# Performance work log

Hardware: AMD Instinct MI355X
Metric: run time of the kernel (lower is better)

The kernel has to match this reference:

```python
import jax, jax.numpy as jnp
import numpy as np

H = 1024

def gru_step(x, h, W_ih, W_hh, b_ih, b_hh):
    # torch.nn.GRUCell math; gate order r, z, n
    gi = x @ W_ih.T + b_ih            # [N, 3H]
    gh = h @ W_hh.T + b_hh            # [N, 3H]
    i_r, i_z, i_n = jnp.split(gi, 3, axis=-1)
    h_r, h_z, h_n = jnp.split(gh, 3, axis=-1)
    r = jax.nn.sigmoid(i_r + h_r)
    z = jax.nn.sigmoid(i_z + h_z)
    n = jnp.tanh(i_n + r * h_n)
    return (1.0 - z) * n + z * h


def setup_inputs() -> dict:
    key = jax.random.key(0)
    ks = jax.random.split(key, 12)
    V, Nr, Na = 256, 4096, 4096
    s = 1.0 / np.sqrt(H)
    return {
        'state': jax.random.normal(ks[0], (1, H), jnp.float32),
        'rel_tokens': jax.random.randint(ks[1], (Nr, 3), 0, V, jnp.int32),
        'attr_tokens': jax.random.randint(ks[2], (Na, 2), 0, V, jnp.int32),
        'table': jax.random.normal(ks[3], (V, H), jnp.float32),
        'W_emb': jax.random.normal(ks[4], (H, H), jnp.float32) * s,
        'b_emb': jnp.zeros((H,), jnp.float32),
        'W_ih': jax.random.normal(ks[5], (3 * H, H), jnp.float32) * s,
        'W_hh': jax.random.normal(ks[6], (3 * H, H), jnp.float32) * s,
        'b_ih': jnp.zeros((3 * H,), jnp.float32),
        'b_hh': jnp.zeros((3 * H,), jnp.float32),
        'W1': jax.random.normal(ks[7], (H, H), jnp.float32) * s,
        'b1': jnp.zeros((H,), jnp.float32),
        'W2': jax.random.normal(ks[8], (H, H), jnp.float32) * s,
        'b2': jnp.zeros((H,), jnp.float32),
        'W3': jax.random.normal(ks[9], (1, H), jnp.float32) * s,
        'b3': jnp.zeros((1,), jnp.float32),
        'eps': jax.random.uniform(ks[10], (1,), jnp.float32) * 0.1,
    }


def reference(state, rel_tokens, attr_tokens, table, W_emb, b_emb,
              W_ih, W_hh, b_ih, b_hh, W1, b1, W2, b2, W3, b3, eps):
    Nr, Na = rel_tokens.shape[0], attr_tokens.shape[0]
    # per-clause token embeddings passed through embedding_layer (Linear)
    rel_e = jnp.einsum('nte,he->nth', table[rel_tokens], W_emb) + b_emb   # [Nr,3,H]
    att_e = jnp.einsum('nte,he->nth', table[attr_tokens], W_emb) + b_emb  # [Na,2,H]

    # relation clauses: 3 chained GRU steps from global state
    h = jnp.broadcast_to(state, (Nr, H))
    for t in range(3):
        h = gru_step(rel_e[:, t], h, W_ih, W_hh, b_ih, b_hh)
    rel_h = h
    # attribute clauses: 2 chained GRU steps from global state
    h = jnp.broadcast_to(state, (Na, H))
    for t in range(2):
        h = gru_step(att_e[:, t], h, W_ih, W_hh, b_ih, b_hh)
    attr_h = h

    clause = jnp.concatenate([rel_h, attr_h], axis=0)          # [N, H]
    x = jax.nn.relu(clause @ W1.T + b1)
    x = jax.nn.relu(x @ W2.T + b2)
    logits = (x @ W3.T + b3).reshape(1, -1)                    # [1, N]
    probs = jax.nn.softmax(logits, axis=1)                     # softmax over clauses
    n = jnp.float32(probs.shape[1])
    probs = probs * (1.0 - eps[0]) + eps[0] / n                # eps smoothing
    return probs
```

## Files before the change

### kernel.cpp

```cpp
#include <hip/hip_runtime.h>
#include <math.h>

#define H 1024
#define H3 3072
#define NVOC 256

typedef __attribute__((ext_vector_type(8))) short bf16x8;
typedef __attribute__((ext_vector_type(4))) float f32x4;

__device__ __forceinline__ float sigf(float x) { return 1.0f / (1.0f + expf(-x)); }

__device__ __forceinline__ unsigned short f2bf(float f) {
    unsigned int u = __float_as_uint(f);
    u = (u + 0x7fffu + ((u >> 16) & 1u)) >> 16;
    return (unsigned short)u;
}
__device__ __forceinline__ float bf2f(unsigned short u) {
    return __uint_as_float(((unsigned int)u) << 16);
}

#define MM256(MH, AV, BV)                                                          \
    __builtin_amdgcn_s_setprio(1);                                                 \
    _Pragma("unroll")                                                              \
    for (int m_ = 0; m_ < 4; ++m_)                                                 \
        _Pragma("unroll")                                                          \
        for (int n_ = 0; n_ < 4; ++n_)                                             \
            acc[(MH) * 4 + m_][n_] = __builtin_amdgcn_mfma_f32_16x16x32_bf16(      \
                AV[m_], BV[n_], acc[(MH) * 4 + m_][n_], 0, 0, 0);                  \
    __builtin_amdgcn_s_setprio(0);

#define RDA256(BUF, MH, KQ)                                                        \
    _Pragma("unroll")                                                              \
    for (int m_ = 0; m_ < 4; ++m_)                                                 \
        a[m_] = *reinterpret_cast<const bf16x8*>(                                  \
            ldsb + (BUF) * 65536 + (g * 128 + (MH) * 64 + m_ * 16 + fr) * 128 +    \
            (((KQ) * 4 + fq) ^ (fr & 7)) * 16);

#define RDB256(BUF, KQ, DST)                                                       \
    _Pragma("unroll")                                                              \
    for (int n_ = 0; n_ < 4; ++n_)                                                 \
        DST[n_] = *reinterpret_cast<const bf16x8*>(                                \
            ldsb + (BUF) * 65536 + 32768 + (wn + n_ * 16 + fr) * 128 +             \
            (((KQ) * 4 + fq) ^ (fr & 7)) * 16);

#define BAR256() __builtin_amdgcn_s_barrier()

template<bool RELU, int OUT_MODE>
__global__ __launch_bounds__(512, 2)
void gemm256(const unsigned short* __restrict__ A, const unsigned short* __restrict__ W,
             const float* __restrict__ bias, void* __restrict__ C,
             int N, int K, int gx,
             const float* __restrict__ w3, float* __restrict__ logits)
{
    __shared__ unsigned short lds[65536];
    char* ldsb = (char*)lds;
    const int tid = threadIdx.x;
    const int wid = tid >> 6, lane = tid & 63;

    const int nwg = gridDim.x;
    const int cpx = nwg >> 3;
    const int bid = blockIdx.x;
    const int swz = (bid & 7) * cpx + (bid >> 3);
    const int bm = (swz / gx) * 256;
    const int bn = (swz % gx) * 256;

    const int g = wid >> 2;
    const int wn = (wid & 3) * 64;
    const int fr = lane & 15, fq = lane >> 4;

    const int sr = tid >> 3;
    const int sc = ((tid & 7) ^ (sr & 7)) * 8;
    auto stage_unit = [&](int t, int u) {
        const unsigned short* src = (u < 4)
            ? A + (size_t)(bm + u * 64 + sr) * K + t * 64 + sc
            : W + (size_t)(bn + (u - 4) * 64 + sr) * K + t * 64 + sc;
        char* dst = ldsb + (t & 1) * 65536 + u * 8192 + tid * 16;
        __builtin_amdgcn_global_load_lds(
            (const __attribute__((address_space(1))) void*)src,
            (__attribute__((address_space(3))) void*)dst, 16, 0, 0);
    };

    f32x4 acc[8][4];
#pragma unroll
    for (int i = 0; i < 8; i++)
#pragma unroll
        for (int j = 0; j < 4; j++) acc[i][j] = (f32x4){0.f, 0.f, 0.f, 0.f};
    bf16x8 a[4], b0[4], b1[4];

    const int nt = K >> 6;

#pragma unroll
    for (int u = 0; u < 8; ++u) stage_unit(0, u);
    stage_unit(1, 0); stage_unit(1, 2); stage_unit(1, 4);
    stage_unit(1, 5); stage_unit(1, 6); stage_unit(1, 7);
    asm volatile("s_waitcnt vmcnt(6)" ::: "memory");
    __builtin_amdgcn_sched_barrier(0);
    BAR256();

    for (int t = 0; t < nt; ++t) {
        const int buf = t & 1;
        RDB256(buf, 0, b0); RDA256(buf, 0, 0);
        if (t + 1 < nt) stage_unit(t + 1, 1);
        MM256(0, a, b0); BAR256();
        RDB256(buf, 1, b1); RDA256(buf, 0, 1);
        if (t + 1 < nt) stage_unit(t + 1, 3);
        MM256(0, a, b1); BAR256();
        RDA256(buf, 1, 0);
        if (t + 2 < nt) { stage_unit(t + 2, 0); stage_unit(t + 2, 2); stage_unit(t + 2, 4); }
        MM256(1, a, b0); BAR256();
        RDA256(buf, 1, 1);
        if (t + 2 < nt) { stage_unit(t + 2, 5); stage_unit(t + 2, 6); stage_unit(t + 2, 7); }
        MM256(1, a, b1);
        if (t + 2 < nt) {
            asm volatile("s_waitcnt vmcnt(6)" ::: "memory");
            __builtin_amdgcn_sched_barrier(0);
        } else if (t + 1 < nt) {
            asm volatile("s_waitcnt vmcnt(0)" ::: "memory");
            __builtin_amdgcn_sched_barrier(0);
        }
        BAR256();
    }

    if (OUT_MODE == 2) {
        float rs[8][4];
#pragma unroll
        for (int m = 0; m < 8; m++)
#pragma unroll
            for (int j = 0; j < 4; j++) rs[m][j] = 0.f;
#pragma unroll
        for (int n = 0; n < 4; n++) {
            const int col = bn + wn + n * 16 + fr;
            const float bv = bias[col];
            const float wv = w3[col];
#pragma unroll
            for (int m = 0; m < 8; m++)
#pragma unroll
                for (int j = 0; j < 4; j++) {
                    float v = acc[m][n][j] + bv;
                    if (RELU) v = fmaxf(v, 0.f);
                    rs[m][j] = fmaf(v, wv, rs[m][j]);
                }
        }
#pragma unroll
        for (int m = 0; m < 8; m++)
#pragma unroll
            for (int j = 0; j < 4; j++) {
                float s = rs[m][j];
                s += __shfl_xor(s, 1); s += __shfl_xor(s, 2);
                s += __shfl_xor(s, 4); s += __shfl_xor(s, 8);
                if (fr == 0) {
                    const int row = bm + g * 128 + (m >> 2) * 64 + (m & 3) * 16 + fq * 4 + j;
                    atomicAdd(logits + row, s);
                }
            }
    } else {
#pragma unroll
        for (int m = 0; m < 8; m++) {
#pragma unroll
            for (int n = 0; n < 4; n++) {
                const int col = bn + wn + n * 16 + fr;
                const float bv = bias[col];
#pragma unroll
                for (int j = 0; j < 4; j++) {
                    const int row = bm + g * 128 + (m >> 2) * 64 + (m & 3) * 16 + fq * 4 + j;
                    float v = acc[m][n][j] + bv;
                    if (RELU) v = fmaxf(v, 0.f);
                    ((unsigned short*)C)[(size_t)row * N + col] = f2bf(v);
                }
            }
        }
    }
}

template<bool RELU, int OUT_MODE>
__global__ __launch_bounds__(256)
void gemm_bf16(const unsigned short* __restrict__ A, const unsigned short* __restrict__ W,
               const float* __restrict__ bias, void* __restrict__ C,
               int N, int K, int gx, int Kc,
               const float* __restrict__ w3, float* __restrict__ logits)
{
    __shared__ unsigned short As[4][128 * 32];
    __shared__ unsigned short Ws[4][128 * 32];
    const int tid = threadIdx.x;
    const int wid = tid >> 6, lane = tid & 63;

    const int nwg = gridDim.x;
    const int cpx = nwg >> 3;
    const int bid = blockIdx.x;
    const int swz = (bid & 7) * cpx + (bid >> 3);
    const int bm = (swz / gx) * 128;
    const int bn = (swz % gx) * 128;
    const int k_base = blockIdx.y * Kc;
    const int nt = Kc >> 5;

    const int wm = (wid >> 1) * 64, wn = (wid & 1) * 64;
    const int fr = lane & 15;
    const int fq = lane >> 4;
    const int perm = fq ^ (fr & 3);

    f32x4 acc[4][4];
#pragma unroll
    for (int i = 0; i < 4; i++)
#pragma unroll
        for (int j = 0; j < 4; j++) acc[i][j] = (f32x4){0.f, 0.f, 0.f, 0.f};

    const int srow = tid >> 2;
    const int schunk = (tid & 3) ^ (srow & 3);
    const unsigned short* aS = A + (size_t)(bm + srow) * K + k_base + schunk * 8;
    const unsigned short* wS = W + (size_t)(bn + srow) * K + k_base + schunk * 8;
    const size_t rstep = (size_t)64 * K;

    auto stage = [&](int b, int t) {
        const unsigned short* a0 = aS + t * 32;
        const unsigned short* w0 = wS + t * 32;
        __builtin_amdgcn_global_load_lds(
            (const __attribute__((address_space(1))) void*)a0,
            (__attribute__((address_space(3))) void*)(&As[b][wid * 512]), 16, 0, 0);
        __builtin_amdgcn_global_load_lds(
            (const __attribute__((address_space(1))) void*)(a0 + rstep),
            (__attribute__((address_space(3))) void*)(&As[b][2048 + wid * 512]), 16, 0, 0);
        __builtin_amdgcn_global_load_lds(
            (const __attribute__((address_space(1))) void*)w0,
            (__attribute__((address_space(3))) void*)(&Ws[b][wid * 512]), 16, 0, 0);
        __builtin_amdgcn_global_load_lds(
            (const __attribute__((address_space(1))) void*)(w0 + rstep),
            (__attribute__((address_space(3))) void*)(&Ws[b][2048 + wid * 512]), 16, 0, 0);
    };

    stage(0, 0);
    if (nt > 1) stage(1, 1);
    if (nt > 2) stage(2, 2);

    for (int t = 0; t < nt; ++t) {
        if (t + 2 < nt)      asm volatile("s_waitcnt vmcnt(8)" ::: "memory");
        else if (t + 1 < nt) asm volatile("s_waitcnt vmcnt(4)" ::: "memory");
        else                 asm volatile("s_waitcnt vmcnt(0)" ::: "memory");
        __builtin_amdgcn_s_barrier();
        __builtin_amdgcn_sched_barrier(0);
        if (t + 3 < nt) stage((t + 3) & 3, t + 3);

        const unsigned short* as = &As[t & 3][0];
        const unsigned short* ws = &Ws[t & 3][0];
        bf16x8 a[4], b[4];
#pragma unroll
        for (int m = 0; m < 4; m++)
            a[m] = *reinterpret_cast<const bf16x8*>(as + (wm + m * 16 + fr) * 32 + perm * 8);
#pragma unroll
        for (int n = 0; n < 4; n++)
            b[n] = *reinterpret_cast<const bf16x8*>(ws + (wn + n * 16 + fr) * 32 + perm * 8);
        __builtin_amdgcn_s_setprio(1);
#pragma unroll
        for (int m = 0; m < 4; m++)
#pragma unroll
            for (int n = 0; n < 4; n++)
                acc[m][n] = __builtin_amdgcn_mfma_f32_16x16x32_bf16(a[m], b[n], acc[m][n], 0, 0, 0);
        __builtin_amdgcn_s_setprio(0);
    }

    if (OUT_MODE == 3) {
        float* Cf = (float*)C;
#pragma unroll
        for (int m = 0; m < 4; m++)
#pragma unroll
            for (int n = 0; n < 4; n++) {
                const int col = bn + wn + n * 16 + fr;
#pragma unroll
                for (int j = 0; j < 4; j++) {
                    const int row = bm + wm + m * 16 + fq * 4 + j;
                    atomicAdd(Cf + (size_t)row * N + col, acc[m][n][j]);
                }
            }
    } else {
#pragma unroll
        for (int m = 0; m < 4; m++) {
#pragma unroll
            for (int n = 0; n < 4; n++) {
                const int col = bn + wn + n * 16 + fr;
                const float bv = bias[col];
#pragma unroll
                for (int j = 0; j < 4; j++) {
                    const int row = bm + wm + m * 16 + fq * 4 + j;
                    float v = acc[m][n][j] + bv;
                    if (RELU) v = fmaxf(v, 0.f);
                    if (OUT_MODE == 1)
                        ((unsigned short*)C)[(size_t)row * N + col] = f2bf(v);
                    else
                        ((float*)C)[(size_t)row * N + col] = v;
                }
            }
        }
    }
}

__global__ __launch_bounds__(256)
void prep(const float* __restrict__ W_hh, const float* __restrict__ W_ih,
          const float* __restrict__ W1, const float* __restrict__ W2,
          const float* __restrict__ W_emb, const float* __restrict__ table,
          const float* __restrict__ state, const float* __restrict__ b_emb,
          const float* __restrict__ b_ih, const float* __restrict__ b_hh,
          unsigned short* __restrict__ W_hhb, unsigned short* __restrict__ W_ihb,
          unsigned short* __restrict__ W1b, unsigned short* __restrict__ W2b,
          unsigned short* __restrict__ W_embb, unsigned short* __restrict__ tableb,
          float* __restrict__ gh0, float* __restrict__ emb32, float* __restrict__ Gi,
          float* __restrict__ gh1, float* __restrict__ logits)
{
    int b = blockIdx.x;
    const int t = threadIdx.x;
    if (b < 3072) {
        float4 w = *reinterpret_cast<const float4*>(W_hh + (size_t)b * H + t * 4);
        ushort4 o; o.x = f2bf(w.x); o.y = f2bf(w.y); o.z = f2bf(w.z); o.w = f2bf(w.w);
        *reinterpret_cast<ushort4*>(W_hhb + (size_t)b * H + t * 4) = o;
        float4 sv = *reinterpret_cast<const float4*>(state + t * 4);
        float s = w.x * sv.x + w.y * sv.y + w.z * sv.z + w.w * sv.w;
#pragma unroll
        for (int off = 32; off; off >>= 1) s += __shfl_down(s, off);
        __shared__ float ps[4];
        if ((t & 63) == 0) ps[t >> 6] = s;
        __syncthreads();
        if (t == 0) gh0[b] = ps[0] + ps[1] + ps[2] + ps[3] + b_hh[b];
        return;
    }
    b -= 3072;
    const float* src = nullptr; unsigned short* dst = nullptr;
    if (b < 3072)      { src = W_ih;  dst = W_ihb; }
    else if ((b -= 3072) < 1024) { src = W1; dst = W1b; }
    else if ((b -= 1024) < 1024) { src = W2; dst = W2b; }
    else if ((b -= 1024) < 1024) { src = W_emb; dst = W_embb; }
    else if ((b -= 1024) < 256)  { src = table; dst = tableb; }
    else {
        b -= 256;
        if (b < 256) {
            int i = b * 1024 + t * 4;
            *reinterpret_cast<float4*>(emb32 + i) =
                *reinterpret_cast<const float4*>(b_emb + (i & (H - 1)));
        } else if ((b -= 256) < 768) {
            int i = b * 1024 + t * 4;
            *reinterpret_cast<float4*>(Gi + i) =
                *reinterpret_cast<const float4*>(b_ih + i % H3);
        } else if ((b -= 768) < 768) {
            int i = b * 1024 + t * 4;
            *reinterpret_cast<float4*>(gh1 + i) =
                *reinterpret_cast<const float4*>(b_hh + i % H3);
        } else {
            b -= 768;
            int i = b * 1024 + t * 4;
            *reinterpret_cast<float4*>(logits + i) = (float4){0.f, 0.f, 0.f, 0.f};
        }
        return;
    }
    const int off = b * 1024 + t * 4;
    float4 v = *reinterpret_cast<const float4*>(src + off);
    ushort4 o; o.x = f2bf(v.x); o.y = f2bf(v.y); o.z = f2bf(v.z); o.w = f2bf(v.w);
    *reinterpret_cast<ushort4*>(dst + off) = o;
}

__global__ void cvt_emb(const float* __restrict__ in, unsigned short* __restrict__ out)
{
    int i = (blockIdx.x * blockDim.x + threadIdx.x) * 4;
    float4 v = *reinterpret_cast<const float4*>(in + i);
    ushort4 o;
    o.x = f2bf(v.x); o.y = f2bf(v.y); o.z = f2bf(v.z); o.w = f2bf(v.w);
    *reinterpret_cast<ushort4*>(out + i) = o;
}

__global__ void h1_combine(const float* __restrict__ Gi, const float* __restrict__ gh0,
                           const float* __restrict__ state, float* __restrict__ h1,
                           unsigned short* __restrict__ h1b)
{
    int idx = blockIdx.x * blockDim.x + threadIdx.x;
    int v = idx >> 10, h = idx & (H - 1);
    const float* g = Gi + (size_t)v * H3;
    float r = sigf(g[h] + gh0[h]);
    float z = sigf(g[H + h] + gh0[H + h]);
    float n = tanhf(fmaf(r, gh0[2 * H + h], g[2 * H + h]));
    float v2 = (1.f - z) * n + z * state[h];
    h1[idx] = v2;
    h1b[idx] = f2bf(v2);
}

__global__ void step2_both(const int* __restrict__ rel, const int* __restrict__ attr, int Nr,
                           const float* __restrict__ Gi, const float* __restrict__ gh1,
                           const float* __restrict__ h1,
                           unsigned short* __restrict__ h2b, unsigned short* __restrict__ attr_out)
{
    int idx = blockIdx.x * blockDim.x + threadIdx.x;
    int row = idx >> 10, h = idx & (H - 1);
    int t0, t1, orow = row;
    unsigned short* dst;
    if (row < Nr) { t0 = rel[row * 3 + 0]; t1 = rel[row * 3 + 1]; dst = h2b; }
    else { orow = row - Nr; t0 = attr[orow * 2 + 0]; t1 = attr[orow * 2 + 1]; dst = attr_out; }
    const float* g = Gi + (size_t)t1 * H3;
    const float* gh = gh1 + (size_t)t0 * H3;
    float r = sigf(g[h] + gh[h]);
    float z = sigf(g[H + h] + gh[H + h]);
    float n = tanhf(fmaf(r, gh[2 * H + h], g[2 * H + h]));
    float v = (1.f - z) * n + z * h1[(size_t)t0 * H + h];
    dst[(size_t)orow * H + h] = f2bf(v);
}

__global__ void step3_rel(const int* __restrict__ toks,
                          const float* __restrict__ Gi, const unsigned short* __restrict__ gh2b,
                          const unsigned short* __restrict__ h2b, unsigned short* __restrict__ outb)
{
    int idx = blockIdx.x * blockDim.x + threadIdx.x;
    int row = idx >> 10, h = idx & (H - 1);
    int t2 = toks[row * 3 + 2];
    const float* g = Gi + (size_t)t2 * H3;
    const unsigned short* gh = gh2b + (size_t)row * H3;
    float r = sigf(g[h] + bf2f(gh[h]));
    float z = sigf(g[H + h] + bf2f(gh[H + h]));
    float n = tanhf(fmaf(r, bf2f(gh[2 * H + h]), g[2 * H + h]));
    outb[idx] = f2bf((1.f - z) * n + z * bf2f(h2b[idx]));
}

__global__ void softmax_eps(const float* __restrict__ logits, const float* __restrict__ epsp,
                            float* __restrict__ out, int N)
{
    __shared__ float smax[16], ssum[16];
    int tid = threadIdx.x;
    int nw = blockDim.x >> 6;
    float m = -INFINITY;
    for (int i = tid; i < N; i += blockDim.x) m = fmaxf(m, logits[i]);
#pragma unroll
    for (int off = 32; off; off >>= 1) m = fmaxf(m, __shfl_down(m, off));
    if ((tid & 63) == 0) smax[tid >> 6] = m;
    __syncthreads();
    float M = smax[0];
    for (int i = 1; i < nw; i++) M = fmaxf(M, smax[i]);
    float s = 0.f;
    for (int i = tid; i < N; i += blockDim.x) s += expf(logits[i] - M);
#pragma unroll
    for (int off = 32; off; off >>= 1) s += __shfl_down(s, off);
    if ((tid & 63) == 0) ssum[tid >> 6] = s;
    __syncthreads();
    float S = 0.f;
    for (int i = 0; i < nw; i++) S += ssum[i];
    float e = epsp[0];
    float mul = (1.f - e) / S;
    float add = e / (float)N;
    for (int i = tid; i < N; i += blockDim.x) out[i] = expf(logits[i] - M) * mul + add;
}

extern "C" void kernel_launch(void* const* d_in, const int* in_sizes, int n_in,
                              void* d_out, int out_size, void* d_ws, size_t ws_size,
                              hipStream_t stream)
{
    const float* state       = (const float*)d_in[0];
    const int*   rel_tokens  = (const int*)d_in[1];
    const int*   attr_tokens = (const int*)d_in[2];
    const float* table       = (const float*)d_in[3];
    const float* W_emb       = (const float*)d_in[4];
    const float* b_emb       = (const float*)d_in[5];
    const float* W_ih        = (const float*)d_in[6];
    const float* W_hh        = (const float*)d_in[7];
    const float* b_ih        = (const float*)d_in[8];
    const float* b_hh        = (const float*)d_in[9];
    const float* W1          = (const float*)d_in[10];
    const float* b1          = (const float*)d_in[11];
    const float* W2          = (const float*)d_in[12];
    const float* b2          = (const float*)d_in[13];
    const float* W3          = (const float*)d_in[14];
    const float* eps         = (const float*)d_in[16];

    const int Nr = in_sizes[1] / 3;
    const int Na = in_sizes[2] / 2;
    const int Ntot = Nr + Na;

    float* ws     = (float*)d_ws;
    float* Gi     = ws;
    float* gh0    = Gi + NVOC * H3;
    float* h1     = gh0 + H3;
    float* gh1    = h1 + NVOC * H;
    float* emb32  = gh1 + NVOC * H3;
    float* logits = emb32 + NVOC * H;
    unsigned short* W_hhb   = (unsigned short*)(logits + Ntot);
    unsigned short* W_ihb   = W_hhb + (size_t)H3 * H;
    unsigned short* W1b     = W_ihb + (size_t)H3 * H;
    unsigned short* W2b     = W1b + (size_t)H * H;
    unsigned short* W_embb  = W2b + (size_t)H * H;
    unsigned short* tableb  = W_embb + (size_t)H * H;
    unsigned short* embb    = tableb + (size_t)NVOC * H;
    unsigned short* h1b     = embb + (size_t)NVOC * H;
    unsigned short* h2b     = h1b + (size_t)NVOC * H;
    unsigned short* gh2b    = h2b + (size_t)Nr * H;
    unsigned short* clauseb = gh2b + (size_t)Nr * H3;
    unsigned short* x1b     = clauseb + (size_t)Ntot * H;

    prep<<<11272, 256, 0, stream>>>(W_hh, W_ih, W1, W2, W_emb, table, state,
                                    b_emb, b_ih, b_hh,
                                    W_hhb, W_ihb, W1b, W2b, W_embb, tableb,
                                    gh0, emb32, Gi, gh1, logits);

    gemm_bf16<false, 3><<<dim3((H / 128) * (NVOC / 128), 4), 256, 0, stream>>>(
        tableb, W_embb, nullptr, emb32, H, H, H / 128, H / 4, nullptr, nullptr);
    cvt_emb<<<NVOC * H / 4 / 256, 256, 0, stream>>>(emb32, embb);
    gemm_bf16<false, 3><<<dim3((H3 / 128) * (NVOC / 128), 4), 256, 0, stream>>>(
        embb, W_ihb, nullptr, Gi, H3, H, H3 / 128, H / 4, nullptr, nullptr);
    h1_combine<<<NVOC * H / 256, 256, 0, stream>>>(Gi, gh0, state, h1, h1b);
    gemm_bf16<false, 3><<<dim3((H3 / 128) * (NVOC / 128), 4), 256, 0, stream>>>(
        h1b, W_hhb, nullptr, gh1, H3, H, H3 / 128, H / 4, nullptr, nullptr);
    step2_both<<<Ntot * (H / 256), 256, 0, stream>>>(rel_tokens, attr_tokens, Nr,
                                                     Gi, gh1, h1, h2b,
                                                     clauseb + (size_t)Nr * H);
    gemm256<false, 1><<<(Nr / 256) * (H3 / 256), 512, 0, stream>>>(
        h2b, W_hhb, b_hh, gh2b, H3, H, H3 / 256, nullptr, nullptr);
    step3_rel<<<Nr * (H / 256), 256, 0, stream>>>(rel_tokens, Gi, gh2b, h2b, clauseb);
    gemm256<true, 1><<<(Ntot / 256) * (H / 256), 512, 0, stream>>>(
        clauseb, W1b, b1, x1b, H, H, H / 256, nullptr, nullptr);
    gemm256<true, 2><<<(Ntot / 256) * (H / 256), 512, 0, stream>>>(
        x1b, W2b, b2, nullptr, H, H, H / 256, W3, logits);
    softmax_eps<<<1, 1024, 0, stream>>>(logits, eps, (float*)d_out, Ntot);
}
```

Baseline: 303.5 us.

## Add 128x256-tile triple-buffered GEMM for the MLP layers

Adds a new gemm_n kernel with 128x256 output tiles, a 64-wide K step, a three-stage LDS ring fed by direct global-to-LDS loads, and XOR-swizzled LDS layout. The two MLP GEMMs (W1 and W2 with the fused W3 logit reduction) now use it instead of the 256x256 gemm256. This doubles the workgroup count for these N=8192, H=1024 GEMMs, aiming to fill more CUs and overlap loads with MFMA. The cost is less reuse per tile and a larger LDS footprint per block.

```diff
diff --git a/kernel.cpp b/kernel.cpp
--- a/kernel.cpp
+++ b/kernel.cpp
@@ -163,6 +163,151 @@
 #pragma unroll
                 for (int j = 0; j < 4; j++) {
                     const int row = bm + g * 128 + (m >> 2) * 64 + (m & 3) * 16 + fq * 4 + j;
+                    float v = acc[m][n][j] + bv;
+                    if (RELU) v = fmaxf(v, 0.f);
+                    ((unsigned short*)C)[(size_t)row * N + col] = f2bf(v);
+                }
+            }
+        }
+    }
+}
+
+template<bool RELU, int OUT_MODE>
+__global__ __launch_bounds__(512, 2)
+void gemm_n(const unsigned short* __restrict__ A, const unsigned short* __restrict__ W,
+            const float* __restrict__ bias, void* __restrict__ C,
+            int N, int K, int gx,
+            const float* __restrict__ w3, float* __restrict__ logits)
+{
+    __shared__ unsigned short lds[73728];
+    char* ldsb = (char*)lds;
+    const int tid = threadIdx.x;
+    const int wid = tid >> 6, lane = tid & 63;
+
+    const int nwg = gridDim.x;
+    const int cpx = nwg >> 3;
+    const int bid = blockIdx.x;
+    const int swz = (bid & 7) * cpx + (bid >> 3);
+    const int bm = (swz / gx) * 128;
+    const int bn = (swz % gx) * 256;
+
+    const int g = wid >> 2;
+    const int wn = (wid & 3) * 64;
+    const int fr = lane & 15, fq = lane >> 4;
+
+    const int sr = tid >> 3;
+    const int sc = ((tid & 7) ^ (sr & 7)) * 8;
+    auto stage_unit = [&](int t, int u) {
+        const unsigned short* src = (u < 2)
+            ? A + (size_t)(bm + u * 64 + sr) * K + t * 64 + sc
+            : W + (size_t)(bn + (u - 2) * 64 + sr) * K + t * 64 + sc;
+        char* dst = ldsb + (t % 3) * 49152 + u * 8192 + tid * 16;
+        __builtin_amdgcn_global_load_lds(
+            (const __attribute__((address_space(1))) void*)src,
+            (__attribute__((address_space(3))) void*)dst, 16, 0, 0);
+    };
+
+    f32x4 acc[4][4];
+#pragma unroll
+    for (int i = 0; i < 4; i++)
+#pragma unroll
+        for (int j = 0; j < 4; j++) acc[i][j] = (f32x4){0.f, 0.f, 0.f, 0.f};
+    bf16x8 a[4], b[4];
+
+    const int nt = K >> 6;
+
+#pragma unroll
+    for (int u = 0; u < 6; ++u) stage_unit(0, u);
+#pragma unroll
+    for (int u = 0; u < 6; ++u) stage_unit(1, u);
+    asm volatile("s_waitcnt vmcnt(6)" ::: "memory");
+    __builtin_amdgcn_sched_barrier(0);
+    __builtin_amdgcn_s_barrier();
+
+    for (int t = 0; t < nt; ++t) {
+        const int buf = (t % 3) * 49152;
+#pragma unroll
+        for (int n_ = 0; n_ < 4; ++n_)
+            b[n_] = *reinterpret_cast<const bf16x8*>(
+                ldsb + buf + 16384 + (wn + n_ * 16 + fr) * 128 + ((fq) ^ (fr & 7)) * 16);
+#pragma unroll
+        for (int m_ = 0; m_ < 4; ++m_)
+            a[m_] = *reinterpret_cast<const bf16x8*>(
+                ldsb + buf + (g * 64 + m_ * 16 + fr) * 128 + ((fq) ^ (fr & 7)) * 16);
+        if (t + 2 < nt) { stage_unit(t + 2, 0); stage_unit(t + 2, 1); stage_unit(t + 2, 2); }
+        __builtin_amdgcn_s_setprio(1);
+#pragma unroll
+        for (int m_ = 0; m_ < 4; ++m_)
+#pragma unroll
+            for (int n_ = 0; n_ < 4; ++n_)
+                acc[m_][n_] = __builtin_amdgcn_mfma_f32_16x16x32_bf16(a[m_], b[n_], acc[m_][n_], 0, 0, 0);
+        __builtin_amdgcn_s_setprio(0);
+        __builtin_amdgcn_s_barrier();
+#pragma unroll
+        for (int n_ = 0; n_ < 4; ++n_)
+            b[n_] = *reinterpret_cast<const bf16x8*>(
+                ldsb + buf + 16384 + (wn + n_ * 16 + fr) * 128 + ((4 + fq) ^ (fr & 7)) * 16);
+#pragma unroll
+        for (int m_ = 0; m_ < 4; ++m_)
+            a[m_] = *reinterpret_cast<const bf16x8*>(
+                ldsb + buf + (g * 64 + m_ * 16 + fr) * 128 + ((4 + fq) ^ (fr & 7)) * 16);
+        if (t + 2 < nt) { stage_unit(t + 2, 3); stage_unit(t + 2, 4); stage_unit(t + 2, 5); }
+        __builtin_amdgcn_s_setprio(1);
+#pragma unroll
+        for (int m_ = 0; m_ < 4; ++m_)
+#pragma unroll
+            for (int n_ = 0; n_ < 4; ++n_)
+                acc[m_][n_] = __builtin_amdgcn_mfma_f32_16x16x32_bf16(a[m_], b[n_], acc[m_][n_], 0, 0, 0);
+        __builtin_amdgcn_s_setprio(0);
+        if (t + 2 < nt) {
+            asm volatile("s_waitcnt vmcnt(6)" ::: "memory");
+            __builtin_amdgcn_sched_barrier(0);
+        } else if (t + 1 < nt) {
+            asm volatile("s_waitcnt vmcnt(0)" ::: "memory");
+            __builtin_amdgcn_sched_barrier(0);
+        }
+        __builtin_amdgcn_s_barrier();
+    }
+
+    if (OUT_MODE == 2) {
+        float rs[4][4];
+#pragma unroll
+        for (int m = 0; m < 4; m++)
+#pragma unroll
+            for (int j = 0; j < 4; j++) rs[m][j] = 0.f;
+#pragma unroll
+        for (int n = 0; n < 4; n++) {
+            const int col = bn + wn + n * 16 + fr;
+            const float bv = bias[col];
+            const float wv = w3[col];
+#pragma unroll
+            for (int m = 0; m < 4; m++)
+#pragma unroll
+                for (int j = 0; j < 4; j++) {
+                    float v = acc[m][n][j] + bv;
+                    if (RELU) v = fmaxf(v, 0.f);
+                    rs[m][j] = fmaf(v, wv, rs[m][j]);
+                }
+        }
+#pragma unroll
+        for (int m = 0; m < 4; m++)
+#pragma unroll
+            for (int j = 0; j < 4; j++) {
+                float s = rs[m][j];
+                s += __shfl_xor(s, 1); s += __shfl_xor(s, 2);
+                s += __shfl_xor(s, 4); s += __shfl_xor(s, 8);
+                if (fr == 0) atomicAdd(logits + bm + g * 64 + m * 16 + fq * 4 + j, s);
+            }
+    } else {
+#pragma unroll
+        for (int m = 0; m < 4; m++) {
+#pragma unroll
+            for (int n = 0; n < 4; n++) {
+                const int col = bn + wn + n * 16 + fr;
+                const float bv = bias[col];
+#pragma unroll
+                for (int j = 0; j < 4; j++) {
+                    const int row = bm + g * 64 + m * 16 + fq * 4 + j;
                     float v = acc[m][n][j] + bv;
                     if (RELU) v = fmaxf(v, 0.f);
                     ((unsigned short*)C)[(size_t)row * N + col] = f2bf(v);
@@ -505,9 +650,9 @@
     gemm256<false, 1><<<(Nr / 256) * (H3 / 256), 512, 0, stream>>>(
         h2b, W_hhb, b_hh, gh2b, H3, H, H3 / 256, nullptr, nullptr);
     step3_rel<<<Nr * (H / 256), 256, 0, stream>>>(rel_tokens, Gi, gh2b, h2b, clauseb);
-    gemm256<true, 1><<<(Ntot / 256) * (H / 256), 512, 0, stream>>>(
+    gemm_n<true, 1><<<(Ntot / 128) * (H / 256), 512, 0, stream>>>(
         clauseb, W1b, b1, x1b, H, H, H / 256, nullptr, nullptr);
-    gemm256<true, 2><<<(Ntot / 256) * (H / 256), 512, 0, stream>>>(
+    gemm_n<true, 2><<<(Ntot / 128) * (H / 256), 512, 0, stream>>>(
         x1b, W2b, b2, nullptr, H, H, H / 256, W3, logits);
     softmax_eps<<<1, 1024, 0, stream>>>(logits, eps, (float*)d_out, Ntot);
 }
```

Measured after the change: 282.0 us. 7.1% less time.
